# Performance work log

Measured on AMD Instinct MI355X. Metric: run time of the kernel, lower is better.

## Reference

```python
import jax, jax.numpy as jnp
import numpy as np

N = 50000      # nodes
E = 800000     # edges (avg degree 16)
D = 3          # dim_world
L = 128        # latent_dim
STEPS = 10     # message passing steps
RID = 64       # num_rigid_ids
REMB = 16      # rigid_embedding_dim


def _mlp2(x, w1, b1, w2, b2):
    # 2-layer MLP: Linear -> ReLU -> Linear (layer_norm=False, dropout=0)
    return jnp.maximum(x @ w1 + b1, 0.0) @ w2 + b2


def setup_inputs() -> dict:
    key = jax.random.key(0)
    ks = jax.random.split(key, 24)
    f32 = jnp.float32

    def lin(k, i, o):
        return (jax.random.normal(k, (i, o), f32) / np.sqrt(i)).astype(f32)

    node_in = 2 * D + 1 + REMB   # 23
    edge_in = 2 * D + 2 + 1      # 9

    receivers = jax.random.randint(ks[4], (E,), 0, N)
    # no self edges (radius_graph uses include_self_edges=False)
    senders = (receivers + jax.random.randint(ks[3], (E,), 1, N)) % N

    inp = {
        'positions': jax.random.uniform(ks[0], (N, D), f32),
        'velocities': jax.random.normal(ks[1], (N, D), f32),
        'rigid_id': jax.random.randint(ks[2], (N,), 0, RID),
        'senders': senders,
        'receivers': receivers,
        'rigid_emb': jax.random.normal(ks[5], (RID, REMB), f32) * 0.1,
        # node encoder
        'ne_w1': lin(ks[6], node_in, L), 'ne_b1': jnp.zeros((L,), f32),
        'ne_w2': lin(ks[7], L, L),       'ne_b2': jnp.zeros((L,), f32),
        # edge encoder
        'ee_w1': lin(ks[8], edge_in, L), 'ee_b1': jnp.zeros((L,), f32),
        'ee_w2': lin(ks[9], L, L),       'ee_b2': jnp.zeros((L,), f32),
        # processor blocks (stacked over STEPS)
        'pe_w1': (jax.random.normal(ks[10], (STEPS, 3 * L, L), f32) / np.sqrt(3 * L)).astype(f32),
        'pe_b1': jnp.zeros((STEPS, L), f32),
        'pe_w2': (jax.random.normal(ks[11], (STEPS, L, L), f32) / np.sqrt(L)).astype(f32),
        'pe_b2': jnp.zeros((STEPS, L), f32),
        'pn_w1': (jax.random.normal(ks[12], (STEPS, 2 * L, L), f32) / np.sqrt(2 * L)).astype(f32),
        'pn_b1': jnp.zeros((STEPS, L), f32),
        'pn_w2': (jax.random.normal(ks[13], (STEPS, L, L), f32) / np.sqrt(L)).astype(f32),
        'pn_b2': jnp.zeros((STEPS, L), f32),
        # decoder (2 layers -> output_dim = D)
        'de_w1': lin(ks[14], L, L), 'de_b1': jnp.zeros((L,), f32),
        'de_w2': lin(ks[15], L, D), 'de_b2': jnp.zeros((D,), f32),
    }
    return inp


def reference(positions, velocities, rigid_id, senders, receivers, rigid_emb,
              ne_w1, ne_b1, ne_w2, ne_b2, ee_w1, ee_b1, ee_w2, ee_b2,
              pe_w1, pe_b1, pe_w2, pe_b2, pn_w1, pn_b1, pn_w2, pn_b2,
              de_w1, de_b1, de_w2, de_b2):
    n = positions.shape[0]
    dt = positions.dtype

    # ----- feature construction (build_gns_graph_inputs + rigid features) -----
    deg = jax.ops.segment_sum(jnp.ones(receivers.shape, dt), receivers, num_segments=n)[:, None]
    center = positions.mean(axis=0, keepdims=True)
    rigid_feat = rigid_emb[rigid_id]                                # [N, REMB]
    node_feat = jnp.concatenate([velocities, positions - center, deg, rigid_feat], axis=-1)

    rel_pos = positions[senders] - positions[receivers]             # [E, D]
    rel_vel = velocities[senders] - velocities[receivers]
    sq = jnp.sum(rel_pos * rel_pos, axis=-1, keepdims=True)
    dist = jnp.sqrt(sq)
    same = (rigid_id[senders] == rigid_id[receivers]).astype(dt)[:, None]
    edge_feat = jnp.concatenate([rel_pos, rel_vel, dist, sq, same], axis=-1)

    # ----- encode -----
    nl = _mlp2(node_feat, ne_w1, ne_b1, ne_w2, ne_b2)               # [N, L]
    el = _mlp2(edge_feat, ee_w1, ee_b1, ee_w2, ee_b2)               # [E, L]

    # ----- process: gather -> edge MLP -> scatter-add -> node MLP, residual -----
    for i in range(pe_w1.shape[0]):
        edge_in = jnp.concatenate([el, nl[senders], nl[receivers]], axis=-1)  # [E, 3L]
        el = el + _mlp2(edge_in, pe_w1[i], pe_b1[i], pe_w2[i], pe_b2[i])
        agg = jax.ops.segment_sum(el, receivers, num_segments=n)              # [N, L]
        node_in = jnp.concatenate([nl, agg], axis=-1)                         # [N, 2L]
        nl = nl + _mlp2(node_in, pn_w1[i], pn_b1[i], pn_w2[i], pn_b2[i])

    # ----- decode -----
    return _mlp2(nl, de_w1, de_b1, de_w2, de_b2)                    # [N, D]
```

## Files before the change

kernel.cpp:

```cpp
#include <hip/hip_runtime.h>
#include <hip/hip_bf16.h>

#define NN 50000
#define NE 800000
#define LDIM 128
#define NSTEPS 10

typedef __hip_bfloat16 bf16;
typedef __bf16 bf8v __attribute__((ext_vector_type(8)));
typedef float f4v __attribute__((ext_vector_type(4)));
typedef unsigned short u16x8 __attribute__((ext_vector_type(8)));

__device__ inline float bflo(unsigned int u) {
    union { unsigned int i; float f; } x; x.i = u << 16; return x.f;
}
__device__ inline float bfhi(unsigned int u) {
    union { unsigned int i; float f; } x; x.i = u & 0xffff0000u; return x.f;
}
__device__ inline unsigned short f2bf(float f) {
    __hip_bfloat16 h = __float2bfloat16(f);
    unsigned short u; __builtin_memcpy(&u, &h, 2); return u;
}


__global__ void k_hist(const int* __restrict__ rcv, int* __restrict__ cnt) {
    int i = blockIdx.x * 256 + threadIdx.x;
    if (i < NE) atomicAdd(&cnt[rcv[i]], 1);
}

__global__ __launch_bounds__(1024) void k_scan(
    const int* __restrict__ cnt, int* __restrict__ row_start,
    int* __restrict__ cur, float* __restrict__ degf) {
    __shared__ int part[1024];
    const int t = threadIdx.x;
    const int CH = (NN + 1023) / 1024;
    int b0 = t * CH, b1 = b0 + CH; if (b1 > NN) b1 = NN; if (b0 > NN) b0 = NN;
    int s = 0;
    for (int i = b0; i < b1; i++) s += cnt[i];
    part[t] = s;
    __syncthreads();
    for (int off = 1; off < 1024; off <<= 1) {
        int v = (t >= off) ? part[t - off] : 0;
        __syncthreads();
        part[t] += v;
        __syncthreads();
    }
    int run = part[t] - s;
    for (int i = b0; i < b1; i++) {
        row_start[i] = run; cur[i] = run; degf[i] = (float)cnt[i];
        run += cnt[i];
    }
    if (t == 1023) row_start[NN] = part[1023];
}

__global__ void k_scatter(const int* __restrict__ snd, const int* __restrict__ rcv,
                          int* __restrict__ cur,
                          unsigned short* __restrict__ snd_p, unsigned short* __restrict__ rcv_p) {
    int i = blockIdx.x * 256 + threadIdx.x;
    if (i < NE) {
        int r = rcv[i];
        int p = atomicAdd(&cur[r], 1);
        snd_p[p] = (unsigned short)snd[i];
        rcv_p[p] = (unsigned short)r;
    }
}

__global__ void k_center(const float* __restrict__ pos, float* __restrict__ csum) {
    __shared__ float s[3][256];
    float a = 0.f, b = 0.f, c = 0.f;
    for (int i = blockIdx.x * 256 + threadIdx.x; i < NN; i += gridDim.x * 256) {
        a += pos[3 * i]; b += pos[3 * i + 1]; c += pos[3 * i + 2];
    }
    int t = threadIdx.x;
    s[0][t] = a; s[1][t] = b; s[2][t] = c;
    __syncthreads();
    for (int off = 128; off > 0; off >>= 1) {
        if (t < off) {
            s[0][t] += s[0][t + off];
            s[1][t] += s[1][t + off];
            s[2][t] += s[2][t + off];
        }
        __syncthreads();
    }
    if (t == 0) {
        atomicAdd(&csum[0], s[0][0]);
        atomicAdd(&csum[1], s[1][0]);
        atomicAdd(&csum[2], s[2][0]);
    }
}


__global__ void k_prep_w(const float* __restrict__ w, unsigned short* __restrict__ wf,
                         int KT, int Ksrc, int lo) {
    int b = blockIdx.x;
    int s = b / (KT * 8), rem = b % (KT * 8);
    int kt = rem / 8, nt = rem % 8;
    int lane = threadIdx.x, col = lane & 15, quad = lane >> 4;
    const float* W = w + (size_t)s * Ksrc * 128;
    u16x8 o;
#pragma unroll
    for (int jj = 0; jj < 8; jj++) {
        int k = kt * 32 + quad * 8 + jj;
        float x = (k < Ksrc) ? W[(size_t)k * 128 + nt * 16 + col] : 0.f;
        unsigned short h = f2bf(x);
        if (lo) h = f2bf(x - bflo(h));
        o[jj] = h;
    }
    *(u16x8*)(wf + (((size_t)b) * 64 + lane) * 8) = o;
}


__global__ __launch_bounds__(256) void k_agg(
    const unsigned short* __restrict__ el, const int* __restrict__ row_start,
    unsigned short* __restrict__ agg) {
    const int wave = threadIdx.x >> 6, lane = threadIdx.x & 63;
    const int n = blockIdx.x * 4 + wave;
    if (n >= NN) return;
    const int sub = lane >> 4, c16 = lane & 15;
    const int st = row_start[n], en = row_start[n + 1];
    float s[8];
#pragma unroll
    for (int k = 0; k < 8; k++) s[k] = 0.f;
    for (int q = st + sub; q < en; q += 4) {
        uint4 v = *(const uint4*)(el + (size_t)q * 128 + c16 * 8);
        s[0] += bflo(v.x); s[1] += bfhi(v.x);
        s[2] += bflo(v.y); s[3] += bfhi(v.y);
        s[4] += bflo(v.z); s[5] += bfhi(v.z);
        s[6] += bflo(v.w); s[7] += bfhi(v.w);
    }
#pragma unroll
    for (int k = 0; k < 8; k++) {
        s[k] += __shfl_xor(s[k], 16);
        s[k] += __shfl_xor(s[k], 32);
    }
    if (sub == 0) {
        u16x8 o;
#pragma unroll
        for (int k = 0; k < 8; k++) o[k] = f2bf(s[k]);
        *(u16x8*)(agg + (size_t)n * 128 + c16 * 8) = o;
    }
}


__global__ __launch_bounds__(256) void k_node_enc_m(
    const float* __restrict__ pos, const float* __restrict__ vel,
    const int* __restrict__ rid, const float* __restrict__ remb,
    const float* __restrict__ degf, const float* __restrict__ csum,
    const unsigned short* __restrict__ w1h, const unsigned short* __restrict__ w1l,
    const float* __restrict__ b1,
    const unsigned short* __restrict__ w2h, const unsigned short* __restrict__ w2l,
    const float* __restrict__ b2,
    unsigned short* __restrict__ nlh, unsigned short* __restrict__ nll) {
    __shared__ __align__(16) unsigned short feat_s[32 * 72];
    __shared__ __align__(16) unsigned short hid_s[32 * 264];
    const int tid = threadIdx.x, wave = tid >> 6, lane = tid & 63;
    const int col = lane & 15, quad = lane >> 4;
    bf8v W1H[2], W1L[2], W2H[4][2], W2L[4][2];
#pragma unroll
    for (int t = 0; t < 2; t++) {
        W1H[t] = *(const bf8v*)(w1h + ((size_t)(2 * wave + t) * 64 + lane) * 8);
        W1L[t] = *(const bf8v*)(w1l + ((size_t)(2 * wave + t) * 64 + lane) * 8);
    }
#pragma unroll
    for (int kt = 0; kt < 4; kt++)
#pragma unroll
        for (int t = 0; t < 2; t++) {
            W2H[kt][t] = *(const bf8v*)(w2h + ((size_t)(kt * 8 + 2 * wave + t) * 64 + lane) * 8);
            W2L[kt][t] = *(const bf8v*)(w2l + ((size_t)(kt * 8 + 2 * wave + t) * 64 + lane) * 8);
        }
    float bias1[2], bias2[2];
#pragma unroll
    for (int t = 0; t < 2; t++) {
        bias1[t] = b1[(2 * wave + t) * 16 + col];
        bias2[t] = b2[(2 * wave + t) * 16 + col];
    }
    float cx = csum[0] * (1.0f / NN), cy = csum[1] * (1.0f / NN), cz = csum[2] * (1.0f / NN);
    uint4 z = {0u, 0u, 0u, 0u};
    for (int s2 = tid; s2 < 288; s2 += 256) *(uint4*)(feat_s + s2 * 8) = z;

    for (int it = 0; it < 4; it++) {
        const int base = blockIdx.x * 128 + it * 32;
        if (base >= NN) break;
        __syncthreads();
        if (tid < 32) {
            int n = base + tid; if (n > NN - 1) n = NN - 1;
            float v[23];
            v[0] = vel[3 * n]; v[1] = vel[3 * n + 1]; v[2] = vel[3 * n + 2];
            v[3] = pos[3 * n] - cx; v[4] = pos[3 * n + 1] - cy; v[5] = pos[3 * n + 2] - cz;
            v[6] = degf[n];
            int rb = rid[n] * 16;
#pragma unroll
            for (int k = 0; k < 16; k++) v[7 + k] = remb[rb + k];
            unsigned short* f = feat_s + tid * 72;
#pragma unroll
            for (int k = 0; k < 23; k++) {
                unsigned short h = f2bf(v[k]);
                f[k] = h; f[32 + k] = f2bf(v[k] - bflo(h));
            }
        }
        __syncthreads();
        f4v acc[2][2];
#pragma unroll
        for (int mt = 0; mt < 2; mt++)
#pragma unroll
            for (int t = 0; t < 2; t++) acc[mt][t] = (f4v){0.f, 0.f, 0.f, 0.f};
        {
            bf8v a0h = *(const bf8v*)(feat_s + col * 72 + quad * 8);
            bf8v a1h = *(const bf8v*)(feat_s + (16 + col) * 72 + quad * 8);
            bf8v a0l = *(const bf8v*)(feat_s + col * 72 + 32 + quad * 8);
            bf8v a1l = *(const bf8v*)(feat_s + (16 + col) * 72 + 32 + quad * 8);
#pragma unroll
            for (int t = 0; t < 2; t++) {
                acc[0][t] = __builtin_amdgcn_mfma_f32_16x16x32_bf16(a0h, W1H[t], acc[0][t], 0, 0, 0);
                acc[1][t] = __builtin_amdgcn_mfma_f32_16x16x32_bf16(a1h, W1H[t], acc[1][t], 0, 0, 0);
                acc[0][t] = __builtin_amdgcn_mfma_f32_16x16x32_bf16(a0l, W1H[t], acc[0][t], 0, 0, 0);
                acc[1][t] = __builtin_amdgcn_mfma_f32_16x16x32_bf16(a1l, W1H[t], acc[1][t], 0, 0, 0);
                acc[0][t] = __builtin_amdgcn_mfma_f32_16x16x32_bf16(a0h, W1L[t], acc[0][t], 0, 0, 0);
                acc[1][t] = __builtin_amdgcn_mfma_f32_16x16x32_bf16(a1h, W1L[t], acc[1][t], 0, 0, 0);
            }
        }
#pragma unroll
        for (int mt = 0; mt < 2; mt++)
#pragma unroll
            for (int t = 0; t < 2; t++) {
                const int nc = (2 * wave + t) * 16 + col;
#pragma unroll
                for (int r = 0; r < 4; r++) {
                    float h = fmaxf(acc[mt][t][r] + bias1[t], 0.f);
                    unsigned short hh = f2bf(h);
                    hid_s[(mt * 16 + quad * 4 + r) * 264 + nc] = hh;
                    hid_s[(mt * 16 + quad * 4 + r) * 264 + 128 + nc] = f2bf(h - bflo(hh));
                }
            }
        __syncthreads();
#pragma unroll
        for (int mt = 0; mt < 2; mt++)
#pragma unroll
            for (int t = 0; t < 2; t++) acc[mt][t] = (f4v){0.f, 0.f, 0.f, 0.f};
#pragma unroll
        for (int kt = 0; kt < 8; kt++) {
            int w = kt & 3;
            bf8v a0 = *(const bf8v*)(hid_s + col * 264 + kt * 32 + quad * 8);
            bf8v a1 = *(const bf8v*)(hid_s + (16 + col) * 264 + kt * 32 + quad * 8);
#pragma unroll
            for (int t = 0; t < 2; t++) {
                acc[0][t] = __builtin_amdgcn_mfma_f32_16x16x32_bf16(a0, W2H[w][t], acc[0][t], 0, 0, 0);
                acc[1][t] = __builtin_amdgcn_mfma_f32_16x16x32_bf16(a1, W2H[w][t], acc[1][t], 0, 0, 0);
            }
        }
#pragma unroll
        for (int kt = 0; kt < 4; kt++) {
            bf8v a0 = *(const bf8v*)(hid_s + col * 264 + kt * 32 + quad * 8);
            bf8v a1 = *(const bf8v*)(hid_s + (16 + col) * 264 + kt * 32 + quad * 8);
#pragma unroll
            for (int t = 0; t < 2; t++) {
                acc[0][t] = __builtin_amdgcn_mfma_f32_16x16x32_bf16(a0, W2L[kt][t], acc[0][t], 0, 0, 0);
                acc[1][t] = __builtin_amdgcn_mfma_f32_16x16x32_bf16(a1, W2L[kt][t], acc[1][t], 0, 0, 0);
            }
        }
        __syncthreads();
#pragma unroll
        for (int mt = 0; mt < 2; mt++)
#pragma unroll
            for (int t = 0; t < 2; t++) {
                const int nc = (2 * wave + t) * 16 + col;
#pragma unroll
                for (int r = 0; r < 4; r++) {
                    const int row = mt * 16 + quad * 4 + r;
                    float v = acc[mt][t][r] + bias2[t];
                    unsigned short hh = f2bf(v);
                    hid_s[row * 264 + nc] = hh;
                    hid_s[row * 264 + 128 + nc] = f2bf(v - bflo(hh));
                }
            }
        __syncthreads();
#pragma unroll
        for (int p = 0; p < 2; p++) {
            int s2 = p * 256 + tid, e = s2 >> 4, c16 = s2 & 15;
            if (base + e < NN) {
                *(uint4*)(nlh + (size_t)(base + e) * 128 + c16 * 8) =
                    *(const uint4*)(hid_s + e * 264 + c16 * 8);
                *(uint4*)(nll + (size_t)(base + e) * 128 + c16 * 8) =
                    *(const uint4*)(hid_s + e * 264 + 128 + c16 * 8);
            }
        }
    }
}


__global__ __launch_bounds__(256) void k_edge_enc_m(
    const float* __restrict__ pos, const float* __restrict__ vel,
    const int* __restrict__ rid,
    const unsigned short* __restrict__ snd, const unsigned short* __restrict__ rcv,
    const unsigned short* __restrict__ w1h, const unsigned short* __restrict__ w1l,
    const float* __restrict__ b1,
    const unsigned short* __restrict__ w2h, const unsigned short* __restrict__ w2l,
    const float* __restrict__ b2,
    unsigned short* __restrict__ el) {
    __shared__ __align__(16) unsigned short feat_s[32 * 72];
    __shared__ __align__(16) unsigned short hid_s[32 * 264];
    const int tid = threadIdx.x, wave = tid >> 6, lane = tid & 63;
    const int col = lane & 15, quad = lane >> 4;
    bf8v W1H[2], W1L[2], W2H[4][2], W2L[4][2];
#pragma unroll
    for (int t = 0; t < 2; t++) {
        W1H[t] = *(const bf8v*)(w1h + ((size_t)(2 * wave + t) * 64 + lane) * 8);
        W1L[t] = *(const bf8v*)(w1l + ((size_t)(2 * wave + t) * 64 + lane) * 8);
    }
#pragma unroll
    for (int kt = 0; kt < 4; kt++)
#pragma unroll
        for (int t = 0; t < 2; t++) {
            W2H[kt][t] = *(const bf8v*)(w2h + ((size_t)(kt * 8 + 2 * wave + t) * 64 + lane) * 8);
            W2L[kt][t] = *(const bf8v*)(w2l + ((size_t)(kt * 8 + 2 * wave + t) * 64 + lane) * 8);
        }
    float bias1[2], bias2[2];
#pragma unroll
    for (int t = 0; t < 2; t++) {
        bias1[t] = b1[(2 * wave + t) * 16 + col];
        bias2[t] = b2[(2 * wave + t) * 16 + col];
    }
    uint4 z = {0u, 0u, 0u, 0u};
    for (int s2 = tid; s2 < 288; s2 += 256) *(uint4*)(feat_s + s2 * 8) = z;

    for (int it = 0; it < 4; it++) {
        const int base = blockIdx.x * 128 + it * 32;
        __syncthreads();
        if (tid < 32) {
            int e = base + tid;
            int s = snd[e], r = rcv[e];
            float v[9];
            v[0] = pos[3 * s] - pos[3 * r]; v[1] = pos[3 * s + 1] - pos[3 * r + 1]; v[2] = pos[3 * s + 2] - pos[3 * r + 2];
            v[3] = vel[3 * s] - vel[3 * r]; v[4] = vel[3 * s + 1] - vel[3 * r + 1]; v[5] = vel[3 * s + 2] - vel[3 * r + 2];
            float sq = v[0] * v[0] + v[1] * v[1] + v[2] * v[2];
            v[6] = sqrtf(sq); v[7] = sq;
            v[8] = (rid[s] == rid[r]) ? 1.f : 0.f;
            unsigned short* f = feat_s + tid * 72;
#pragma unroll
            for (int k = 0; k < 9; k++) {
                unsigned short h = f2bf(v[k]);
                f[k] = h; f[32 + k] = f2bf(v[k] - bflo(h));
            }
        }
        __syncthreads();
        f4v acc[2][2];
#pragma unroll
        for (int mt = 0; mt < 2; mt++)
#pragma unroll
            for (int t = 0; t < 2; t++) acc[mt][t] = (f4v){0.f, 0.f, 0.f, 0.f};
        {
            bf8v a0h = *(const bf8v*)(feat_s + col * 72 + quad * 8);
            bf8v a1h = *(const bf8v*)(feat_s + (16 + col) * 72 + quad * 8);
            bf8v a0l = *(const bf8v*)(feat_s + col * 72 + 32 + quad * 8);
            bf8v a1l = *(const bf8v*)(feat_s + (16 + col) * 72 + 32 + quad * 8);
#pragma unroll
            for (int t = 0; t < 2; t++) {
                acc[0][t] = __builtin_amdgcn_mfma_f32_16x16x32_bf16(a0h, W1H[t], acc[0][t], 0, 0, 0);
                acc[1][t] = __builtin_amdgcn_mfma_f32_16x16x32_bf16(a1h, W1H[t], acc[1][t], 0, 0, 0);
                acc[0][t] = __builtin_amdgcn_mfma_f32_16x16x32_bf16(a0l, W1H[t], acc[0][t], 0, 0, 0);
                acc[1][t] = __builtin_amdgcn_mfma_f32_16x16x32_bf16(a1l, W1H[t], acc[1][t], 0, 0, 0);
                acc[0][t] = __builtin_amdgcn_mfma_f32_16x16x32_bf16(a0h, W1L[t], acc[0][t], 0, 0, 0);
                acc[1][t] = __builtin_amdgcn_mfma_f32_16x16x32_bf16(a1h, W1L[t], acc[1][t], 0, 0, 0);
            }
        }
#pragma unroll
        for (int mt = 0; mt < 2; mt++)
#pragma unroll
            for (int t = 0; t < 2; t++) {
                const int nc = (2 * wave + t) * 16 + col;
#pragma unroll
                for (int r = 0; r < 4; r++) {
                    float h = fmaxf(acc[mt][t][r] + bias1[t], 0.f);
                    unsigned short hh = f2bf(h);
                    hid_s[(mt * 16 + quad * 4 + r) * 264 + nc] = hh;
                    hid_s[(mt * 16 + quad * 4 + r) * 264 + 128 + nc] = f2bf(h - bflo(hh));
                }
            }
        __syncthreads();
#pragma unroll
        for (int mt = 0; mt < 2; mt++)
#pragma unroll
            for (int t = 0; t < 2; t++) acc[mt][t] = (f4v){0.f, 0.f, 0.f, 0.f};
#pragma unroll
        for (int kt = 0; kt < 8; kt++) {
            int w = kt & 3;
            bf8v a0 = *(const bf8v*)(hid_s + col * 264 + kt * 32 + quad * 8);
            bf8v a1 = *(const bf8v*)(hid_s + (16 + col) * 264 + kt * 32 + quad * 8);
#pragma unroll
            for (int t = 0; t < 2; t++) {
                acc[0][t] = __builtin_amdgcn_mfma_f32_16x16x32_bf16(a0, W2H[w][t], acc[0][t], 0, 0, 0);
                acc[1][t] = __builtin_amdgcn_mfma_f32_16x16x32_bf16(a1, W2H[w][t], acc[1][t], 0, 0, 0);
            }
        }
#pragma unroll
        for (int kt = 0; kt < 4; kt++) {
            bf8v a0 = *(const bf8v*)(hid_s + col * 264 + kt * 32 + quad * 8);
            bf8v a1 = *(const bf8v*)(hid_s + (16 + col) * 264 + kt * 32 + quad * 8);
#pragma unroll
            for (int t = 0; t < 2; t++) {
                acc[0][t] = __builtin_amdgcn_mfma_f32_16x16x32_bf16(a0, W2L[kt][t], acc[0][t], 0, 0, 0);
                acc[1][t] = __builtin_amdgcn_mfma_f32_16x16x32_bf16(a1, W2L[kt][t], acc[1][t], 0, 0, 0);
            }
        }
        __syncthreads();
#pragma unroll
        for (int mt = 0; mt < 2; mt++)
#pragma unroll
            for (int t = 0; t < 2; t++) {
                const int nc = (2 * wave + t) * 16 + col;
#pragma unroll
                for (int r = 0; r < 4; r++)
                    hid_s[(mt * 16 + quad * 4 + r) * 264 + nc] = f2bf(acc[mt][t][r] + bias2[t]);
            }
        __syncthreads();
#pragma unroll
        for (int p = 0; p < 2; p++) {
            int s2 = p * 256 + tid, e = s2 >> 4, c16 = s2 & 15;
            *(uint4*)(el + (size_t)(base + e) * 128 + c16 * 8) =
                *(const uint4*)(hid_s + e * 264 + c16 * 8);
        }
    }
}


__global__ __launch_bounds__(256) void k_edge_step(
    unsigned short* __restrict__ el, const unsigned short* __restrict__ nlh,
    const unsigned short* __restrict__ snd, const unsigned short* __restrict__ rcv,
    const unsigned short* __restrict__ w1f, const float* __restrict__ b1,
    const unsigned short* __restrict__ w2f, const float* __restrict__ b2) {
    __shared__ __align__(16) unsigned short inl_s[32 * 392];
    __shared__ __align__(16) unsigned short hid_s[32 * 136];
    const int tid = threadIdx.x;
    const int wave = tid >> 6, lane = tid & 63;
    const int col = lane & 15, quad = lane >> 4;
    const int erow = tid >> 4, c16 = tid & 15;

    bf8v W1[12][2], W2[4][2];
#pragma unroll
    for (int kt = 0; kt < 12; kt++)
#pragma unroll
        for (int t = 0; t < 2; t++)
            W1[kt][t] = *(const bf8v*)(w1f + ((size_t)(kt * 8 + 2 * wave + t) * 64 + lane) * 8);
#pragma unroll
    for (int kt = 0; kt < 4; kt++)
#pragma unroll
        for (int t = 0; t < 2; t++)
            W2[kt][t] = *(const bf8v*)(w2f + ((size_t)(kt * 8 + 2 * wave + t) * 64 + lane) * 8);
    float bias1[2], bias2[2];
#pragma unroll
    for (int t = 0; t < 2; t++) {
        bias1[t] = b1[(2 * wave + t) * 16 + col];
        bias2[t] = b2[(2 * wave + t) * 16 + col];
    }

    uint4 pf_s[2];
#pragma unroll
    for (int p = 0; p < 2; p++) {
        int ge = blockIdx.x * 256 + p * 16 + erow;
        pf_s[p] = *(const uint4*)(nlh + (size_t)snd[ge] * 128 + c16 * 8);
    }

    for (int it = 0; it < 8; it++) {
        const int base = blockIdx.x * 256 + it * 32;
        __syncthreads();
#pragma unroll
        for (int p = 0; p < 2; p++) {
            int e = p * 16 + erow;
            int ge = base + e;
            *(uint4*)(inl_s + e * 392 + c16 * 8) =
                *(const uint4*)(el + (size_t)ge * 128 + c16 * 8);
            *(uint4*)(inl_s + e * 392 + 128 + c16 * 8) = pf_s[p];
            *(uint4*)(inl_s + e * 392 + 256 + c16 * 8) =
                *(const uint4*)(nlh + (size_t)rcv[ge] * 128 + c16 * 8);
        }
        if (it < 7) {
#pragma unroll
            for (int p = 0; p < 2; p++) {
                int ge = base + 32 + p * 16 + erow;
                pf_s[p] = *(const uint4*)(nlh + (size_t)snd[ge] * 128 + c16 * 8);
            }
        }
        __syncthreads();

        f4v acc[2][2];
#pragma unroll
        for (int mt = 0; mt < 2; mt++)
#pragma unroll
            for (int t = 0; t < 2; t++) acc[mt][t] = (f4v){0.f, 0.f, 0.f, 0.f};
#pragma unroll
        for (int kt = 0; kt < 12; kt++) {
            bf8v a0 = *(const bf8v*)(inl_s + col * 392 + kt * 32 + quad * 8);
            bf8v a1 = *(const bf8v*)(inl_s + (16 + col) * 392 + kt * 32 + quad * 8);
            acc[0][0] = __builtin_amdgcn_mfma_f32_16x16x32_bf16(a0, W1[kt][0], acc[0][0], 0, 0, 0);
            acc[0][1] = __builtin_amdgcn_mfma_f32_16x16x32_bf16(a0, W1[kt][1], acc[0][1], 0, 0, 0);
            acc[1][0] = __builtin_amdgcn_mfma_f32_16x16x32_bf16(a1, W1[kt][0], acc[1][0], 0, 0, 0);
            acc[1][1] = __builtin_amdgcn_mfma_f32_16x16x32_bf16(a1, W1[kt][1], acc[1][1], 0, 0, 0);
        }
#pragma unroll
        for (int mt = 0; mt < 2; mt++)
#pragma unroll
            for (int t = 0; t < 2; t++) {
                const int nc = (2 * wave + t) * 16 + col;
#pragma unroll
                for (int r = 0; r < 4; r++) {
                    float v = fmaxf(acc[mt][t][r] + bias1[t], 0.f);
                    hid_s[(mt * 16 + quad * 4 + r) * 136 + nc] = f2bf(v);
                }
            }
        __syncthreads();

#pragma unroll
        for (int mt = 0; mt < 2; mt++)
#pragma unroll
            for (int t = 0; t < 2; t++) acc[mt][t] = (f4v){0.f, 0.f, 0.f, 0.f};
#pragma unroll
        for (int kt = 0; kt < 4; kt++) {
            bf8v a0 = *(const bf8v*)(hid_s + col * 136 + kt * 32 + quad * 8);
            bf8v a1 = *(const bf8v*)(hid_s + (16 + col) * 136 + kt * 32 + quad * 8);
            acc[0][0] = __builtin_amdgcn_mfma_f32_16x16x32_bf16(a0, W2[kt][0], acc[0][0], 0, 0, 0);
            acc[0][1] = __builtin_amdgcn_mfma_f32_16x16x32_bf16(a0, W2[kt][1], acc[0][1], 0, 0, 0);
            acc[1][0] = __builtin_amdgcn_mfma_f32_16x16x32_bf16(a1, W2[kt][0], acc[1][0], 0, 0, 0);
            acc[1][1] = __builtin_amdgcn_mfma_f32_16x16x32_bf16(a1, W2[kt][1], acc[1][1], 0, 0, 0);
        }
        __syncthreads();
#pragma unroll
        for (int mt = 0; mt < 2; mt++)
#pragma unroll
            for (int t = 0; t < 2; t++) {
                const int nc = (2 * wave + t) * 16 + col;
#pragma unroll
                for (int r = 0; r < 4; r++) {
                    const int row = mt * 16 + quad * 4 + r;
                    float v = acc[mt][t][r] + bias2[t] + bflo((unsigned int)inl_s[row * 392 + nc]);
                    hid_s[row * 136 + nc] = f2bf(v);
                }
            }
        __syncthreads();
#pragma unroll
        for (int p = 0; p < 2; p++) {
            int e = p * 16 + erow;
            *(uint4*)(el + (size_t)(base + e) * 128 + c16 * 8) =
                *(const uint4*)(hid_s + e * 136 + c16 * 8);
        }
    }
}


__global__ __launch_bounds__(256) void k_node_step_s(
    unsigned short* __restrict__ nlh, unsigned short* __restrict__ nll,
    const unsigned short* __restrict__ agg,
    const unsigned short* __restrict__ w1h, const unsigned short* __restrict__ w1l,
    const float* __restrict__ b1,
    const unsigned short* __restrict__ w2h, const unsigned short* __restrict__ w2l,
    const float* __restrict__ b2) {
    __shared__ __align__(16) unsigned short a_s[32 * 392];
    __shared__ __align__(16) unsigned short hid_s[32 * 264];
    const int tid = threadIdx.x, wave = tid >> 6, lane = tid & 63;
    const int col = lane & 15, quad = lane >> 4;
    bf8v W1H[8][2], W1L[8][2], W2H[4][2], W2L[4][2];
#pragma unroll
    for (int kt = 0; kt < 8; kt++)
#pragma unroll
        for (int t = 0; t < 2; t++) {
            W1H[kt][t] = *(const bf8v*)(w1h + ((size_t)(kt * 8 + 2 * wave + t) * 64 + lane) * 8);
            W1L[kt][t] = *(const bf8v*)(w1l + ((size_t)(kt * 8 + 2 * wave + t) * 64 + lane) * 8);
        }
#pragma unroll
    for (int kt = 0; kt < 4; kt++)
#pragma unroll
        for (int t = 0; t < 2; t++) {
            W2H[kt][t] = *(const bf8v*)(w2h + ((size_t)(kt * 8 + 2 * wave + t) * 64 + lane) * 8);
            W2L[kt][t] = *(const bf8v*)(w2l + ((size_t)(kt * 8 + 2 * wave + t) * 64 + lane) * 8);
        }
    float bias1[2], bias2[2];
#pragma unroll
    for (int t = 0; t < 2; t++) {
        bias1[t] = b1[(2 * wave + t) * 16 + col];
        bias2[t] = b2[(2 * wave + t) * 16 + col];
    }
    for (int it = 0; it < 2; it++) {
        const int base = blockIdx.x * 64 + it * 32;
        if (base >= NN) break;
        __syncthreads();
#pragma unroll
        for (int p = 0; p < 2; p++) {
            int e = p * 16 + (tid >> 4), c16 = tid & 15;
            int n = base + e; if (n > NN - 1) n = NN - 1;
            *(uint4*)(a_s + e * 392 + c16 * 8) =
                *(const uint4*)(nlh + (size_t)n * 128 + c16 * 8);
            *(uint4*)(a_s + e * 392 + 128 + c16 * 8) =
                *(const uint4*)(nll + (size_t)n * 128 + c16 * 8);
            *(uint4*)(a_s + e * 392 + 256 + c16 * 8) =
                *(const uint4*)(agg + (size_t)n * 128 + c16 * 8);
        }
        __syncthreads();

        f4v acc[2][2];
#pragma unroll
        for (int mt = 0; mt < 2; mt++)
#pragma unroll
            for (int t = 0; t < 2; t++) acc[mt][t] = (f4v){0.f, 0.f, 0.f, 0.f};
#pragma unroll
        for (int kt = 0; kt < 8; kt++) {
            bf8v a0 = *(const bf8v*)(a_s + col * 392 + kt * 32 + quad * 8);
            bf8v a1 = *(const bf8v*)(a_s + (16 + col) * 392 + kt * 32 + quad * 8);
#pragma unroll
            for (int t = 0; t < 2; t++) {
                acc[0][t] = __builtin_amdgcn_mfma_f32_16x16x32_bf16(a0, W1H[kt & 3][t], acc[0][t], 0, 0, 0);
                acc[1][t] = __builtin_amdgcn_mfma_f32_16x16x32_bf16(a1, W1H[kt & 3][t], acc[1][t], 0, 0, 0);
            }
        }
#pragma unroll
        for (int kt = 0; kt < 4; kt++) {
            bf8v a0 = *(const bf8v*)(a_s + col * 392 + 256 + kt * 32 + quad * 8);
            bf8v a1 = *(const bf8v*)(a_s + (16 + col) * 392 + 256 + kt * 32 + quad * 8);
#pragma unroll
            for (int t = 0; t < 2; t++) {
                acc[0][t] = __builtin_amdgcn_mfma_f32_16x16x32_bf16(a0, W1H[4 + kt][t], acc[0][t], 0, 0, 0);
                acc[1][t] = __builtin_amdgcn_mfma_f32_16x16x32_bf16(a1, W1H[4 + kt][t], acc[1][t], 0, 0, 0);
            }
        }
#pragma unroll
        for (int kt = 0; kt < 4; kt++) {
            bf8v a0 = *(const bf8v*)(a_s + col * 392 + kt * 32 + quad * 8);
            bf8v a1 = *(const bf8v*)(a_s + (16 + col) * 392 + kt * 32 + quad * 8);
#pragma unroll
            for (int t = 0; t < 2; t++) {
                acc[0][t] = __builtin_amdgcn_mfma_f32_16x16x32_bf16(a0, W1L[kt][t], acc[0][t], 0, 0, 0);
                acc[1][t] = __builtin_amdgcn_mfma_f32_16x16x32_bf16(a1, W1L[kt][t], acc[1][t], 0, 0, 0);
            }
        }
#pragma unroll
        for (int kt = 0; kt < 4; kt++) {
            bf8v a0 = *(const bf8v*)(a_s + col * 392 + 256 + kt * 32 + quad * 8);
            bf8v a1 = *(const bf8v*)(a_s + (16 + col) * 392 + 256 + kt * 32 + quad * 8);
#pragma unroll
            for (int t = 0; t < 2; t++) {
                acc[0][t] = __builtin_amdgcn_mfma_f32_16x16x32_bf16(a0, W1L[4 + kt][t], acc[0][t], 0, 0, 0);
                acc[1][t] = __builtin_amdgcn_mfma_f32_16x16x32_bf16(a1, W1L[4 + kt][t], acc[1][t], 0, 0, 0);
            }
        }
#pragma unroll
        for (int mt = 0; mt < 2; mt++)
#pragma unroll
            for (int t = 0; t < 2; t++) {
                const int nc = (2 * wave + t) * 16 + col;
#pragma unroll
                for (int r = 0; r < 4; r++) {
                    float h = fmaxf(acc[mt][t][r] + bias1[t], 0.f);
                    unsigned short hh = f2bf(h);
                    hid_s[(mt * 16 + quad * 4 + r) * 264 + nc] = hh;
                    hid_s[(mt * 16 + quad * 4 + r) * 264 + 128 + nc] = f2bf(h - bflo(hh));
                }
            }
        __syncthreads();
#pragma unroll
        for (int mt = 0; mt < 2; mt++)
#pragma unroll
            for (int t = 0; t < 2; t++) acc[mt][t] = (f4v){0.f, 0.f, 0.f, 0.f};
#pragma unroll
        for (int kt = 0; kt < 8; kt++) {
            int w = kt & 3;
            bf8v a0 = *(const bf8v*)(hid_s + col * 264 + kt * 32 + quad * 8);
            bf8v a1 = *(const bf8v*)(hid_s + (16 + col) * 264 + kt * 32 + quad * 8);
#pragma unroll
            for (int t = 0; t < 2; t++) {
                acc[0][t] = __builtin_amdgcn_mfma_f32_16x16x32_bf16(a0, W2H[w][t], acc[0][t], 0, 0, 0);
                acc[1][t] = __builtin_amdgcn_mfma_f32_16x16x32_bf16(a1, W2H[w][t], acc[1][t], 0, 0, 0);
            }
        }
#pragma unroll
        for (int kt = 0; kt < 4; kt++) {
            bf8v a0 = *(const bf8v*)(hid_s + col * 264 + kt * 32 + quad * 8);
            bf8v a1 = *(const bf8v*)(hid_s + (16 + col) * 264 + kt * 32 + quad * 8);
#pragma unroll
            for (int t = 0; t < 2; t++) {
                acc[0][t] = __builtin_amdgcn_mfma_f32_16x16x32_bf16(a0, W2L[kt][t], acc[0][t], 0, 0, 0);
                acc[1][t] = __builtin_amdgcn_mfma_f32_16x16x32_bf16(a1, W2L[kt][t], acc[1][t], 0, 0, 0);
            }
        }
        __syncthreads();
#pragma unroll
        for (int mt = 0; mt < 2; mt++)
#pragma unroll
            for (int t = 0; t < 2; t++) {
                const int nc = (2 * wave + t) * 16 + col;
#pragma unroll
                for (int r = 0; r < 4; r++) {
                    const int row = mt * 16 + quad * 4 + r;
                    float res = bflo((unsigned int)a_s[row * 392 + nc]) +
                                bflo((unsigned int)a_s[row * 392 + 128 + nc]);
                    float v = acc[mt][t][r] + bias2[t] + res;
                    unsigned short hh = f2bf(v);
                    hid_s[row * 264 + nc] = hh;
                    hid_s[row * 264 + 128 + nc] = f2bf(v - bflo(hh));
                }
            }
        __syncthreads();
#pragma unroll
        for (int p = 0; p < 2; p++) {
            int e = p * 16 + (tid >> 4), c16 = tid & 15;
            if (base + e < NN) {
                *(uint4*)(nlh + (size_t)(base + e) * 128 + c16 * 8) =
                    *(const uint4*)(hid_s + e * 264 + c16 * 8);
                *(uint4*)(nll + (size_t)(base + e) * 128 + c16 * 8) =
                    *(const uint4*)(hid_s + e * 264 + 128 + c16 * 8);
            }
        }
    }
}


__global__ __launch_bounds__(128) void k_decode(
    const unsigned short* __restrict__ nlh, const unsigned short* __restrict__ nll,
    const float* __restrict__ w1, const float* __restrict__ b1,
    const float* __restrict__ w2, const float* __restrict__ b2,
    float* __restrict__ out) {
    __shared__ float inl[16][128];
    __shared__ float hid[16][128];
    int j = threadIdx.x;
    int base = blockIdx.x * 16;
    for (int e = 0; e < 16; e++)
        inl[e][j] = bflo((unsigned int)nlh[(size_t)(base + e) * 128 + j]) +
                    bflo((unsigned int)nll[(size_t)(base + e) * 128 + j]);
    __syncthreads();
    float acc[16];
#pragma unroll
    for (int e = 0; e < 16; e++) acc[e] = b1[j];
    for (int kc = 0; kc < 16; kc++) {
        float w[8];
#pragma unroll
        for (int t = 0; t < 8; t++) w[t] = w1[(kc * 8 + t) * 128 + j];
#pragma unroll
        for (int e = 0; e < 16; e++) {
            float4 h0 = *(const float4*)&inl[e][kc * 8];
            float4 h1 = *(const float4*)&inl[e][kc * 8 + 4];
            acc[e] = fmaf(h0.x, w[0], acc[e]); acc[e] = fmaf(h0.y, w[1], acc[e]);
            acc[e] = fmaf(h0.z, w[2], acc[e]); acc[e] = fmaf(h0.w, w[3], acc[e]);
            acc[e] = fmaf(h1.x, w[4], acc[e]); acc[e] = fmaf(h1.y, w[5], acc[e]);
            acc[e] = fmaf(h1.z, w[6], acc[e]); acc[e] = fmaf(h1.w, w[7], acc[e]);
        }
    }
#pragma unroll
    for (int e = 0; e < 16; e++) hid[e][j] = fmaxf(acc[e], 0.f);
    __syncthreads();
    if (j < 48) {
        int e = j / 3, ch = j - 3 * (j / 3);
        float s = b2[ch];
        for (int k = 0; k < 128; k++) s = fmaf(hid[e][k], w2[k * 3 + ch], s);
        out[(size_t)(base + e) * 3 + ch] = s;
    }
}


extern "C" void kernel_launch(void* const* d_in, const int* in_sizes, int n_in,
                              void* d_out, int out_size, void* d_ws, size_t ws_size,
                              hipStream_t stream) {
    (void)in_sizes; (void)n_in; (void)out_size; (void)ws_size;
    const float* pos   = (const float*)d_in[0];
    const float* vel   = (const float*)d_in[1];
    const int*   rid   = (const int*)d_in[2];
    const int*   snd   = (const int*)d_in[3];
    const int*   rcv   = (const int*)d_in[4];
    const float* remb  = (const float*)d_in[5];
    const float* ne_w1 = (const float*)d_in[6];
    const float* ne_b1 = (const float*)d_in[7];
    const float* ne_w2 = (const float*)d_in[8];
    const float* ne_b2 = (const float*)d_in[9];
    const float* ee_w1 = (const float*)d_in[10];
    const float* ee_b1 = (const float*)d_in[11];
    const float* ee_w2 = (const float*)d_in[12];
    const float* ee_b2 = (const float*)d_in[13];
    const float* pe_w1 = (const float*)d_in[14];
    const float* pe_b1 = (const float*)d_in[15];
    const float* pe_w2 = (const float*)d_in[16];
    const float* pe_b2 = (const float*)d_in[17];
    const float* pn_w1 = (const float*)d_in[18];
    const float* pn_b1 = (const float*)d_in[19];
    const float* pn_w2 = (const float*)d_in[20];
    const float* pn_b2 = (const float*)d_in[21];
    const float* de_w1 = (const float*)d_in[22];
    const float* de_b1 = (const float*)d_in[23];
    const float* de_w2 = (const float*)d_in[24];
    const float* de_b2 = (const float*)d_in[25];
    float* out = (float*)d_out;

    char* p = (char*)d_ws;
    auto carve = [&](size_t bytes) { void* q = (void*)p; p += (bytes + 15) & ~(size_t)15; return q; };
    unsigned short* el    = (unsigned short*)carve((size_t)NE * LDIM * 2);
    unsigned short* nlh   = (unsigned short*)carve((size_t)NN * LDIM * 2);
    unsigned short* nll   = (unsigned short*)carve((size_t)NN * LDIM * 2);
    unsigned short* agg   = (unsigned short*)carve((size_t)NN * LDIM * 2);
    unsigned short* w1f_e = (unsigned short*)carve((size_t)NSTEPS * 12 * 8 * 512 * 2);
    unsigned short* w2f_e = (unsigned short*)carve((size_t)NSTEPS * 4 * 8 * 512 * 2);
    unsigned short* w1h_n = (unsigned short*)carve((size_t)NSTEPS * 8 * 8 * 512 * 2);
    unsigned short* w1l_n = (unsigned short*)carve((size_t)NSTEPS * 8 * 8 * 512 * 2);
    unsigned short* w2h_n = (unsigned short*)carve((size_t)NSTEPS * 4 * 8 * 512 * 2);
    unsigned short* w2l_n = (unsigned short*)carve((size_t)NSTEPS * 4 * 8 * 512 * 2);
    unsigned short* eew1h = (unsigned short*)carve((size_t)1 * 8 * 512 * 2);
    unsigned short* eew1l = (unsigned short*)carve((size_t)1 * 8 * 512 * 2);
    unsigned short* eew2h = (unsigned short*)carve((size_t)4 * 8 * 512 * 2);
    unsigned short* eew2l = (unsigned short*)carve((size_t)4 * 8 * 512 * 2);
    unsigned short* new1h = (unsigned short*)carve((size_t)1 * 8 * 512 * 2);
    unsigned short* new1l = (unsigned short*)carve((size_t)1 * 8 * 512 * 2);
    unsigned short* new2h = (unsigned short*)carve((size_t)4 * 8 * 512 * 2);
    unsigned short* new2l = (unsigned short*)carve((size_t)4 * 8 * 512 * 2);
    unsigned short* snd_p = (unsigned short*)carve((size_t)NE * 2);
    unsigned short* rcv_p = (unsigned short*)carve((size_t)NE * 2);
    int*            rs    = (int*)carve((size_t)(NN + 1) * 4);
    int*            cnt   = (int*)carve((size_t)NN * 4);
    int*            cur   = (int*)carve((size_t)NN * 4);
    float*          degf  = (float*)carve((size_t)NN * 4);
    float*          csum  = (float*)carve(16);

    hipMemsetAsync(cnt, 0, (size_t)NN * 4, stream);
    hipMemsetAsync(csum, 0, 16, stream);
    k_hist<<<NE / 256, 256, 0, stream>>>(rcv, cnt);
    k_scan<<<1, 1024, 0, stream>>>(cnt, rs, cur, degf);
    k_center<<<64, 256, 0, stream>>>(pos, csum);
    k_scatter<<<NE / 256, 256, 0, stream>>>(snd, rcv, cur, snd_p, rcv_p);
    k_prep_w<<<NSTEPS * 12 * 8, 64, 0, stream>>>(pe_w1, w1f_e, 12, 384, 0);
    k_prep_w<<<NSTEPS * 4 * 8, 64, 0, stream>>>(pe_w2, w2f_e, 4, 128, 0);
    k_prep_w<<<NSTEPS * 8 * 8, 64, 0, stream>>>(pn_w1, w1h_n, 8, 256, 0);
    k_prep_w<<<NSTEPS * 8 * 8, 64, 0, stream>>>(pn_w1, w1l_n, 8, 256, 1);
    k_prep_w<<<NSTEPS * 4 * 8, 64, 0, stream>>>(pn_w2, w2h_n, 4, 128, 0);
    k_prep_w<<<NSTEPS * 4 * 8, 64, 0, stream>>>(pn_w2, w2l_n, 4, 128, 1);
    k_prep_w<<<8, 64, 0, stream>>>(ee_w1, eew1h, 1, 9, 0);
    k_prep_w<<<8, 64, 0, stream>>>(ee_w1, eew1l, 1, 9, 1);
    k_prep_w<<<4 * 8, 64, 0, stream>>>(ee_w2, eew2h, 4, 128, 0);
    k_prep_w<<<4 * 8, 64, 0, stream>>>(ee_w2, eew2l, 4, 128, 1);
    k_prep_w<<<8, 64, 0, stream>>>(ne_w1, new1h, 1, 23, 0);
    k_prep_w<<<8, 64, 0, stream>>>(ne_w1, new1l, 1, 23, 1);
    k_prep_w<<<4 * 8, 64, 0, stream>>>(ne_w2, new2h, 4, 128, 0);
    k_prep_w<<<4 * 8, 64, 0, stream>>>(ne_w2, new2l, 4, 128, 1);

    k_node_enc_m<<<(NN + 127) / 128, 256, 0, stream>>>(pos, vel, rid, remb, degf, csum,
                                                       new1h, new1l, ne_b1, new2h, new2l, ne_b2, nlh, nll);
    k_edge_enc_m<<<NE / 128, 256, 0, stream>>>(pos, vel, rid, snd_p, rcv_p,
                                               eew1h, eew1l, ee_b1, eew2h, eew2l, ee_b2, el);
    for (int i = 0; i < NSTEPS; i++) {
        k_edge_step<<<NE / 256, 256, 0, stream>>>(el, nlh, snd_p, rcv_p,
            w1f_e + (size_t)i * 12 * 8 * 512, pe_b1 + i * 128,
            w2f_e + (size_t)i * 4 * 8 * 512, pe_b2 + i * 128);
        k_agg<<<(NN + 3) / 4, 256, 0, stream>>>(el, rs, agg);
        k_node_step_s<<<(NN + 63) / 64, 256, 0, stream>>>(nlh, nll, agg,
            w1h_n + (size_t)i * 8 * 8 * 512, w1l_n + (size_t)i * 8 * 8 * 512, pn_b1 + i * 128,
            w2h_n + (size_t)i * 4 * 8 * 512, w2l_n + (size_t)i * 4 * 8 * 512, pn_b2 + i * 128);
    }
    k_decode<<<NN / 16, 128, 0, stream>>>(nlh, nll, de_w1, de_b1, de_w2, de_b2, out);
}
```

Measured before the change: 2.924 ms.

## Use 512-thread blocks in edge step with one column tile per wave

The edge-step kernel now runs with 512 threads (8 waves), each wave owning one 16-column output tile instead of two. This halves the per-wave register-resident weight fragments and accumulators so more waves fit per CU, and each thread loads one gathered edge row instead of two. The software prefetch of sender rows is dropped, so gather latency must now be hidden by the extra waves rather than explicit prefetching.

```diff
diff --git a/kernel.cpp b/kernel.cpp
--- a/kernel.cpp
+++ b/kernel.cpp
@@ -423,7 +423,7 @@
 }
 
 
-__global__ __launch_bounds__(256) void k_edge_step(
+__global__ __launch_bounds__(512) void k_edge_step(
     unsigned short* __restrict__ el, const unsigned short* __restrict__ nlh,
     const unsigned short* __restrict__ snd, const unsigned short* __restrict__ rcv,
     const unsigned short* __restrict__ w1f, const float* __restrict__ b1,
@@ -435,113 +435,70 @@
     const int col = lane & 15, quad = lane >> 4;
     const int erow = tid >> 4, c16 = tid & 15;
 
-    bf8v W1[12][2], W2[4][2];
+    bf8v W1[12], W2[4];
 #pragma unroll
     for (int kt = 0; kt < 12; kt++)
-#pragma unroll
-        for (int t = 0; t < 2; t++)
-            W1[kt][t] = *(const bf8v*)(w1f + ((size_t)(kt * 8 + 2 * wave + t) * 64 + lane) * 8);
+        W1[kt] = *(const bf8v*)(w1f + ((size_t)(kt * 8 + wave) * 64 + lane) * 8);
 #pragma unroll
     for (int kt = 0; kt < 4; kt++)
-#pragma unroll
-        for (int t = 0; t < 2; t++)
-            W2[kt][t] = *(const bf8v*)(w2f + ((size_t)(kt * 8 + 2 * wave + t) * 64 + lane) * 8);
-    float bias1[2], bias2[2];
-#pragma unroll
-    for (int t = 0; t < 2; t++) {
-        bias1[t] = b1[(2 * wave + t) * 16 + col];
-        bias2[t] = b2[(2 * wave + t) * 16 + col];
-    }
-
-    uint4 pf_s[2];
-#pragma unroll
-    for (int p = 0; p < 2; p++) {
-        int ge = blockIdx.x * 256 + p * 16 + erow;
-        pf_s[p] = *(const uint4*)(nlh + (size_t)snd[ge] * 128 + c16 * 8);
-    }
+        W2[kt] = *(const bf8v*)(w2f + ((size_t)(kt * 8 + wave) * 64 + lane) * 8);
+    const float bias1 = b1[wave * 16 + col];
+    const float bias2 = b2[wave * 16 + col];
+    const int nc = wave * 16 + col;
 
     for (int it = 0; it < 8; it++) {
         const int base = blockIdx.x * 256 + it * 32;
         __syncthreads();
-#pragma unroll
-        for (int p = 0; p < 2; p++) {
-            int e = p * 16 + erow;
-            int ge = base + e;
-            *(uint4*)(inl_s + e * 392 + c16 * 8) =
+        {
+            int ge = base + erow;
+            *(uint4*)(inl_s + erow * 392 + c16 * 8) =
                 *(const uint4*)(el + (size_t)ge * 128 + c16 * 8);
-            *(uint4*)(inl_s + e * 392 + 128 + c16 * 8) = pf_s[p];
-            *(uint4*)(inl_s + e * 392 + 256 + c16 * 8) =
+            *(uint4*)(inl_s + erow * 392 + 128 + c16 * 8) =
+                *(const uint4*)(nlh + (size_t)snd[ge] * 128 + c16 * 8);
+            *(uint4*)(inl_s + erow * 392 + 256 + c16 * 8) =
                 *(const uint4*)(nlh + (size_t)rcv[ge] * 128 + c16 * 8);
         }
-        if (it < 7) {
-#pragma unroll
-            for (int p = 0; p < 2; p++) {
-                int ge = base + 32 + p * 16 + erow;
-                pf_s[p] = *(const uint4*)(nlh + (size_t)snd[ge] * 128 + c16 * 8);
-            }
-        }
-        __syncthreads();
-
-        f4v acc[2][2];
-#pragma unroll
-        for (int mt = 0; mt < 2; mt++)
-#pragma unroll
-            for (int t = 0; t < 2; t++) acc[mt][t] = (f4v){0.f, 0.f, 0.f, 0.f};
+        __syncthreads();
+
+        f4v acc[2];
+        acc[0] = (f4v){0.f, 0.f, 0.f, 0.f};
+        acc[1] = (f4v){0.f, 0.f, 0.f, 0.f};
 #pragma unroll
         for (int kt = 0; kt < 12; kt++) {
             bf8v a0 = *(const bf8v*)(inl_s + col * 392 + kt * 32 + quad * 8);
             bf8v a1 = *(const bf8v*)(inl_s + (16 + col) * 392 + kt * 32 + quad * 8);
-            acc[0][0] = __builtin_amdgcn_mfma_f32_16x16x32_bf16(a0, W1[kt][0], acc[0][0], 0, 0, 0);
-            acc[0][1] = __builtin_amdgcn_mfma_f32_16x16x32_bf16(a0, W1[kt][1], acc[0][1], 0, 0, 0);
-            acc[1][0] = __builtin_amdgcn_mfma_f32_16x16x32_bf16(a1, W1[kt][0], acc[1][0], 0, 0, 0);
-            acc[1][1] = __builtin_amdgcn_mfma_f32_16x16x32_bf16(a1, W1[kt][1], acc[1][1], 0, 0, 0);
-        }
-#pragma unroll
-        for (int mt = 0; mt < 2; mt++)
-#pragma unroll
-            for (int t = 0; t < 2; t++) {
-                const int nc = (2 * wave + t) * 16 + col;
-#pragma unroll
-                for (int r = 0; r < 4; r++) {
-                    float v = fmaxf(acc[mt][t][r] + bias1[t], 0.f);
-                    hid_s[(mt * 16 + quad * 4 + r) * 136 + nc] = f2bf(v);
-                }
-            }
-        __syncthreads();
-
-#pragma unroll
-        for (int mt = 0; mt < 2; mt++)
-#pragma unroll
-            for (int t = 0; t < 2; t++) acc[mt][t] = (f4v){0.f, 0.f, 0.f, 0.f};
+            acc[0] = __builtin_amdgcn_mfma_f32_16x16x32_bf16(a0, W1[kt], acc[0], 0, 0, 0);
+            acc[1] = __builtin_amdgcn_mfma_f32_16x16x32_bf16(a1, W1[kt], acc[1], 0, 0, 0);
+        }
+#pragma unroll
+        for (int mt = 0; mt < 2; mt++)
+#pragma unroll
+            for (int r = 0; r < 4; r++)
+                hid_s[(mt * 16 + quad * 4 + r) * 136 + nc] =
+                    f2bf(fmaxf(acc[mt][r] + bias1, 0.f));
+        __syncthreads();
+
+        acc[0] = (f4v){0.f, 0.f, 0.f, 0.f};
+        acc[1] = (f4v){0.f, 0.f, 0.f, 0.f};
 #pragma unroll
         for (int kt = 0; kt < 4; kt++) {
             bf8v a0 = *(const bf8v*)(hid_s + col * 136 + kt * 32 + quad * 8);
             bf8v a1 = *(const bf8v*)(hid_s + (16 + col) * 136 + kt * 32 + quad * 8);
-            acc[0][0] = __builtin_amdgcn_mfma_f32_16x16x32_bf16(a0, W2[kt][0], acc[0][0], 0, 0, 0);
-            acc[0][1] = __builtin_amdgcn_mfma_f32_16x16x32_bf16(a0, W2[kt][1], acc[0][1], 0, 0, 0);
-            acc[1][0] = __builtin_amdgcn_mfma_f32_16x16x32_bf16(a1, W2[kt][0], acc[1][0], 0, 0, 0);
-            acc[1][1] = __builtin_amdgcn_mfma_f32_16x16x32_bf16(a1, W2[kt][1], acc[1][1], 0, 0, 0);
-        }
-        __syncthreads();
-#pragma unroll
-        for (int mt = 0; mt < 2; mt++)
-#pragma unroll
-            for (int t = 0; t < 2; t++) {
-                const int nc = (2 * wave + t) * 16 + col;
-#pragma unroll
-                for (int r = 0; r < 4; r++) {
-                    const int row = mt * 16 + quad * 4 + r;
-                    float v = acc[mt][t][r] + bias2[t] + bflo((unsigned int)inl_s[row * 392 + nc]);
-                    hid_s[row * 136 + nc] = f2bf(v);
-                }
-            }
-        __syncthreads();
-#pragma unroll
-        for (int p = 0; p < 2; p++) {
-            int e = p * 16 + erow;
-            *(uint4*)(el + (size_t)(base + e) * 128 + c16 * 8) =
-                *(const uint4*)(hid_s + e * 136 + c16 * 8);
-        }
+            acc[0] = __builtin_amdgcn_mfma_f32_16x16x32_bf16(a0, W2[kt], acc[0], 0, 0, 0);
+            acc[1] = __builtin_amdgcn_mfma_f32_16x16x32_bf16(a1, W2[kt], acc[1], 0, 0, 0);
+        }
+        __syncthreads();
+#pragma unroll
+        for (int mt = 0; mt < 2; mt++)
+#pragma unroll
+            for (int r = 0; r < 4; r++) {
+                const int row = mt * 16 + quad * 4 + r;
+                float v = acc[mt][r] + bias2 + bflo((unsigned int)inl_s[row * 392 + nc]);
+                hid_s[row * 136 + nc] = f2bf(v);
+            }
+        __syncthreads();
+        *(uint4*)(el + (size_t)(base + erow) * 128 + c16 * 8) =
+            *(const uint4*)(hid_s + erow * 136 + c16 * 8);
     }
 }
 
@@ -839,7 +796,7 @@
     k_edge_enc_m<<<NE / 128, 256, 0, stream>>>(pos, vel, rid, snd_p, rcv_p,
                                                eew1h, eew1l, ee_b1, eew2h, eew2l, ee_b2, el);
     for (int i = 0; i < NSTEPS; i++) {
-        k_edge_step<<<NE / 256, 256, 0, stream>>>(el, nlh, snd_p, rcv_p,
+        k_edge_step<<<NE / 256, 512, 0, stream>>>(el, nlh, snd_p, rcv_p,
             w1f_e + (size_t)i * 12 * 8 * 512, pe_b1 + i * 128,
             w2f_e + (size_t)i * 4 * 8 * 512, pe_b2 + i * 128);
         k_agg<<<(NN + 3) / 4, 256, 0, stream>>>(el, rs, agg);
```

New measurement: 2.938 ms. No clear change (+0.5%).
